# Kernel tuning notes

Hardware: AMD Instinct MI355X
Metric: run time of the kernel (lower is better)

The kernel has to match this reference:

```python
import jax, jax.numpy as jnp
import numpy as np

LMAX = 3
D_IN = 16    # sum(2l+1) for l=0..3
D_OUT = 156  # sum over the 34 CG instructions of (2*l3+1)


def _build_sparse_cg():
    """Build the concatenated sparse CG index lists (mu1, mu2, mu3) and
    coefficients, mirroring TensorProduct.__init__: loop over all
    (l1, l2, l3) paths with l3 <= LMAX, take nonzeros of the real-basis
    Wigner-3j tensor (nonzero pattern: |m1' +- m2'| == |m3'|), offset the
    indices by the per-irrep block offsets, and concatenate.
    Coefficient values are deterministic synthetic stand-ins with the
    correct sparsity structure and component-normalization scale."""
    rs = np.random.RandomState(0)
    off_in = [0, 1, 4, 9]  # block offsets for l = 0..3 (block dim 2l+1)
    mu1, mu2, mu3, vals = [], [], [], []
    off3 = 0
    for l1 in range(LMAX + 1):
        for l2 in range(LMAX + 1):
            for l3 in range(abs(l1 - l2), min(l1 + l2, LMAX) + 1):
                for m1 in range(2 * l1 + 1):
                    for m2 in range(2 * l2 + 1):
                        a, b = m1 - l1, m2 - l2
                        for m3 in range(2 * l3 + 1):
                            c = m3 - l3
                            if abs(a + b) == abs(c) or abs(a - b) == abs(c):
                                mu1.append(off_in[l1] + m1)
                                mu2.append(off_in[l2] + m2)
                                mu3.append(off3 + m3)
                                vals.append(rs.randn() / np.sqrt(2 * l3 + 1))
                off3 += 2 * l3 + 1
    assert off3 == D_OUT
    return (np.asarray(mu1, np.int32), np.asarray(mu2, np.int32),
            np.asarray(mu3, np.int32), np.asarray(vals, np.float32))


def setup_inputs() -> dict:
    key = jax.random.key(0)
    k1, k2 = jax.random.split(key)
    B, C = 1024, 128
    x = jax.random.normal(k1, (B, D_IN, C), dtype=jnp.float32)
    y = jax.random.normal(k2, (B, D_IN, C), dtype=jnp.float32)
    mu1, mu2, mu3, cg = _build_sparse_cg()
    return {
        "x": x,
        "y": y,
        "cg": jnp.asarray(cg),
        "mu1": jnp.asarray(mu1),
        "mu2": jnp.asarray(mu2),
        "mu3": jnp.asarray(mu3),
    }


def reference(x, y, cg, mu1, mu2, mu3):
    # Fused equivalent of the per-batch / per-instruction Python loops:
    # out[b, mu3[k], c] += cg[k] * x[b, mu1[k], c] * y[b, mu2[k], c]
    terms = x[:, mu1, :] * cg[None, :, None] * y[:, mu2, :]  # [B, K, C]
    out = jnp.zeros((x.shape[0], D_OUT, x.shape[2]), dtype=x.dtype)
    return out.at[:, mu3, :].add(terms)
```

## Files before the change

kernel.cpp:

```cpp
#include <hip/hip_runtime.h>
#include <utility>


#define D_IN_ 16
#define D_OUT_ 156
#define C_ 128
#define KMAX_ 2048

struct CGRows {
    int n;
    int start[D_OUT_ + 1];
    int k[KMAX_];
    int m1[KMAX_];
    int m2[KMAX_];
};

constexpr CGRows build_rows() {
    int mu1[KMAX_] = {}, mu2[KMAX_] = {}, mu3[KMAX_] = {};
    int n = 0;
    const int off_in[4] = {0, 1, 4, 9};
    int off3 = 0;
    for (int l1 = 0; l1 <= 3; ++l1) {
        for (int l2 = 0; l2 <= 3; ++l2) {
            int lo = l1 > l2 ? l1 - l2 : l2 - l1;
            int hi = (l1 + l2) < 3 ? (l1 + l2) : 3;
            for (int l3 = lo; l3 <= hi; ++l3) {
                for (int m1 = 0; m1 < 2 * l1 + 1; ++m1) {
                    for (int m2 = 0; m2 < 2 * l2 + 1; ++m2) {
                        int a = m1 - l1, b = m2 - l2;
                        for (int m3 = 0; m3 < 2 * l3 + 1; ++m3) {
                            int c = m3 - l3;
                            int s = a + b; if (s < 0) s = -s;
                            int d = a - b; if (d < 0) d = -d;
                            int e = c < 0 ? -c : c;
                            if (s == e || d == e) {
                                mu1[n] = off_in[l1] + m1;
                                mu2[n] = off_in[l2] + m2;
                                mu3[n] = off3 + m3;
                                ++n;
                            }
                        }
                    }
                }
                off3 += 2 * l3 + 1;
            }
        }
    }
    CGRows r{};
    r.n = n;
    int cnt[D_OUT_] = {};
    for (int i = 0; i < n; ++i) cnt[mu3[i]]++;
    r.start[0] = 0;
    for (int j = 0; j < D_OUT_; ++j) r.start[j + 1] = r.start[j] + cnt[j];
    int pos[D_OUT_] = {};
    for (int j = 0; j < D_OUT_; ++j) pos[j] = r.start[j];
    for (int i = 0; i < n; ++i) {
        int j = mu3[i];
        int p = pos[j]++;
        r.k[p] = i;
        r.m1[p] = mu1[i];
        r.m2[p] = mu2[i];
    }
    return r;
}

constexpr CGRows CG = build_rows();

template <int Base, int... Ts>
__device__ __forceinline__ float row_sum_impl(const float* __restrict__ cg,
                                              const float (&xv)[D_IN_],
                                              const float (&yv)[D_IN_],
                                              std::integer_sequence<int, Ts...>) {
    float s = 0.0f;
    ((s = fmaf(cg[CG.k[Base + Ts]], xv[CG.m1[Base + Ts]] * yv[CG.m2[Base + Ts]], s)), ...);
    return s;
}

template <int J>
__device__ __forceinline__ float row_sum(const float* __restrict__ cg,
                                         const float (&xv)[D_IN_],
                                         const float (&yv)[D_IN_]) {
    constexpr int base = CG.start[J];
    constexpr int nt = CG.start[J + 1] - CG.start[J];
    return row_sum_impl<base>(cg, xv, yv, std::make_integer_sequence<int, nt>{});
}

template <int... Js>
__device__ __forceinline__ void all_rows(float* __restrict__ ob,
                                         const float* __restrict__ cg,
                                         const float (&xv)[D_IN_],
                                         const float (&yv)[D_IN_],
                                         std::integer_sequence<int, Js...>) {
    ((ob[Js * C_] = row_sum<Js>(cg, xv, yv)), ...);
}

__global__ __launch_bounds__(256) void tp_cg_kernel(
    const float* __restrict__ x, const float* __restrict__ y,
    const float* __restrict__ cg, float* __restrict__ out) {
    const int c = threadIdx.x & (C_ - 1);
    const int b = (int)((blockIdx.x << 1) | (threadIdx.x >> 7));

    const float* xb = x + (size_t)b * (D_IN_ * C_) + c;
    const float* yb = y + (size_t)b * (D_IN_ * C_) + c;

    float xv[D_IN_], yv[D_IN_];
#pragma unroll
    for (int i = 0; i < D_IN_; ++i) {
        xv[i] = xb[i * C_];
        yv[i] = yb[i * C_];
    }

    float* ob = out + (size_t)b * (D_OUT_ * C_) + c;
    all_rows(ob, cg, xv, yv, std::make_integer_sequence<int, D_OUT_>{});
}

extern "C" void kernel_launch(void* const* d_in, const int* in_sizes, int n_in,
                              void* d_out, int out_size, void* d_ws, size_t ws_size,
                              hipStream_t stream) {
    const float* x  = (const float*)d_in[0];
    const float* y  = (const float*)d_in[1];
    const float* cg = (const float*)d_in[2];
    float* out = (float*)d_out;

    const int B = in_sizes[0] / (D_IN_ * C_);
    const int nblocks = (B * C_) / 256;

    tp_cg_kernel<<<nblocks, 256, 0, stream>>>(x, y, cg, out);
}
```

Baseline: 111.9 us.

## Vectorize to float2 channels, split output rows across wave halves, pre-gather CG

Each thread now handles two adjacent channels with float2 loads and stores. Each batch's output rows are split between two 64-thread halves, and each half loads only the input components its rows need. A small pre-kernel permutes the CG coefficients into row-sorted order in workspace, so the main kernel reads them contiguously instead of through indirect indices. The launch also requests two blocks per CU. The cost is an extra kernel launch, duplicated input loads across the two halves, and both branches inlined into one large kernel.

Measured after the change: 109.5 us. -2.1%, faster.

```diff
diff --git a/kernel.cpp b/kernel.cpp
--- a/kernel.cpp
+++ b/kernel.cpp
@@ -65,53 +65,97 @@
 }
 
 constexpr CGRows CG = build_rows();
+constexpr int K = CG.n;
+static_assert(K <= KMAX_, "KMAX too small");
+
+constexpr int find_split() {
+    int j = 0;
+    while (CG.start[j] < CG.n / 2) ++j;
+    return j;
+}
+constexpr int RSPLIT = find_split();
+
+constexpr unsigned need1(int j0, int j1) {
+    unsigned m = 0;
+    for (int p = CG.start[j0]; p < CG.start[j1]; ++p) m |= 1u << CG.m1[p];
+    return m;
+}
+constexpr unsigned need2(int j0, int j1) {
+    unsigned m = 0;
+    for (int p = CG.start[j0]; p < CG.start[j1]; ++p) m |= 1u << CG.m2[p];
+    return m;
+}
+
+__device__ __constant__ CGRows dCG = build_rows();
+
+__global__ void gather_cg(const float* __restrict__ cg, float* __restrict__ cgs) {
+    int i = blockIdx.x * 256 + threadIdx.x;
+    if (i < K) cgs[i] = cg[dCG.k[i]];
+}
+
+template <unsigned M, int I>
+__device__ __forceinline__ void load1(float2 (&v)[D_IN_], const float* __restrict__ base) {
+    if constexpr ((M >> I) & 1u) v[I] = *(const float2*)(base + I * C_);
+    else v[I] = make_float2(0.0f, 0.0f);
+}
+
+template <unsigned M, int... Is>
+__device__ __forceinline__ void load_masked(float2 (&v)[D_IN_], const float* __restrict__ base,
+                                            std::integer_sequence<int, Is...>) {
+    (load1<M, Is>(v, base), ...);
+}
 
 template <int Base, int... Ts>
-__device__ __forceinline__ float row_sum_impl(const float* __restrict__ cg,
-                                              const float (&xv)[D_IN_],
-                                              const float (&yv)[D_IN_],
-                                              std::integer_sequence<int, Ts...>) {
-    float s = 0.0f;
-    ((s = fmaf(cg[CG.k[Base + Ts]], xv[CG.m1[Base + Ts]] * yv[CG.m2[Base + Ts]], s)), ...);
+__device__ __forceinline__ float2 row_sum2(const float* __restrict__ cgs,
+                                           const float2 (&xv)[D_IN_],
+                                           const float2 (&yv)[D_IN_],
+                                           std::integer_sequence<int, Ts...>) {
+    float2 s = make_float2(0.0f, 0.0f);
+    (((s.x = fmaf(cgs[Base + Ts], xv[CG.m1[Base + Ts]].x * yv[CG.m2[Base + Ts]].x, s.x)),
+      (s.y = fmaf(cgs[Base + Ts], xv[CG.m1[Base + Ts]].y * yv[CG.m2[Base + Ts]].y, s.y))), ...);
     return s;
 }
 
 template <int J>
-__device__ __forceinline__ float row_sum(const float* __restrict__ cg,
-                                         const float (&xv)[D_IN_],
-                                         const float (&yv)[D_IN_]) {
+__device__ __forceinline__ void store_row(float* __restrict__ ob, const float* __restrict__ cgs,
+                                          const float2 (&xv)[D_IN_], const float2 (&yv)[D_IN_]) {
     constexpr int base = CG.start[J];
     constexpr int nt = CG.start[J + 1] - CG.start[J];
-    return row_sum_impl<base>(cg, xv, yv, std::make_integer_sequence<int, nt>{});
+    float2 s = row_sum2<base>(cgs, xv, yv, std::make_integer_sequence<int, nt>{});
+    *(float2*)(ob + J * C_) = s;
 }
 
-template <int... Js>
-__device__ __forceinline__ void all_rows(float* __restrict__ ob,
-                                         const float* __restrict__ cg,
-                                         const float (&xv)[D_IN_],
-                                         const float (&yv)[D_IN_],
-                                         std::integer_sequence<int, Js...>) {
-    ((ob[Js * C_] = row_sum<Js>(cg, xv, yv)), ...);
+template <int J0, int... Js>
+__device__ __forceinline__ void rows_range(float* __restrict__ ob, const float* __restrict__ cgs,
+                                           const float2 (&xv)[D_IN_], const float2 (&yv)[D_IN_],
+                                           std::integer_sequence<int, Js...>) {
+    (store_row<J0 + Js>(ob, cgs, xv, yv), ...);
 }
 
-__global__ __launch_bounds__(256) void tp_cg_kernel(
+__global__ __launch_bounds__(256, 2) void tp_cg_kernel(
     const float* __restrict__ x, const float* __restrict__ y,
-    const float* __restrict__ cg, float* __restrict__ out) {
-    const int c = threadIdx.x & (C_ - 1);
-    const int b = (int)((blockIdx.x << 1) | (threadIdx.x >> 7));
+    const float* __restrict__ cgs, float* __restrict__ out) {
+    const int tid = (int)threadIdx.x;
+    const int c2 = tid & 63;
+    const int half = (tid >> 6) & 1;
+    const int b = (int)((blockIdx.x << 1) | (tid >> 7));
 
-    const float* xb = x + (size_t)b * (D_IN_ * C_) + c;
-    const float* yb = y + (size_t)b * (D_IN_ * C_) + c;
+    const float* xb = x + (size_t)b * (D_IN_ * C_) + c2 * 2;
+    const float* yb = y + (size_t)b * (D_IN_ * C_) + c2 * 2;
+    float* ob = out + (size_t)b * (D_OUT_ * C_) + c2 * 2;
 
-    float xv[D_IN_], yv[D_IN_];
-#pragma unroll
-    for (int i = 0; i < D_IN_; ++i) {
-        xv[i] = xb[i * C_];
-        yv[i] = yb[i * C_];
+    float2 xv[D_IN_], yv[D_IN_];
+    if (half == 0) {
+        constexpr unsigned m1 = need1(0, RSPLIT), m2 = need2(0, RSPLIT);
+        load_masked<m1>(xv, xb, std::make_integer_sequence<int, D_IN_>{});
+        load_masked<m2>(yv, yb, std::make_integer_sequence<int, D_IN_>{});
+        rows_range<0>(ob, cgs, xv, yv, std::make_integer_sequence<int, RSPLIT>{});
+    } else {
+        constexpr unsigned m1 = need1(RSPLIT, D_OUT_), m2 = need2(RSPLIT, D_OUT_);
+        load_masked<m1>(xv, xb, std::make_integer_sequence<int, D_IN_>{});
+        load_masked<m2>(yv, yb, std::make_integer_sequence<int, D_IN_>{});
+        rows_range<RSPLIT>(ob, cgs, xv, yv, std::make_integer_sequence<int, D_OUT_ - RSPLIT>{});
     }
-
-    float* ob = out + (size_t)b * (D_OUT_ * C_) + c;
-    all_rows(ob, cg, xv, yv, std::make_integer_sequence<int, D_OUT_>{});
 }
 
 extern "C" void kernel_launch(void* const* d_in, const int* in_sizes, int n_in,
@@ -121,9 +165,12 @@
     const float* y  = (const float*)d_in[1];
     const float* cg = (const float*)d_in[2];
     float* out = (float*)d_out;
+    float* cgs = (float*)d_ws;
 
     const int B = in_sizes[0] / (D_IN_ * C_);
-    const int nblocks = (B * C_) / 256;
 
-    tp_cg_kernel<<<nblocks, 256, 0, stream>>>(x, y, cg, out);
+    gather_cg<<<(K + 255) / 256, 256, 0, stream>>>(cg, cgs);
+
+    const int nblocks = B / 2;
+    tp_cg_kernel<<<nblocks, 256, 0, stream>>>(x, y, cgs, out);
 }
```

## Split output rows across thread halves by octants, one block per batch

Applied to the files above, without the earlier changes.

Before, each thread computed all 156 output rows for one (batch, channel). Now each block handles a single batch, and its two 128-thread halves each compute four of eight octants of rows, which are balanced by term count. The octant order is rotated by batch index to spread the store pattern, and launch bounds request 4 blocks per CU. This doubles the grid and halves per-thread serial work to improve latency hiding, at the cost of every thread loading the full x/y vectors twice per batch and a runtime switch over octant code.

Result: slower. 294.2 us (+163.0%).

```diff
diff --git a/kernel.cpp b/kernel.cpp
--- a/kernel.cpp
+++ b/kernel.cpp
@@ -65,53 +65,87 @@
 }
 
 constexpr CGRows CG = build_rows();
+constexpr int K = CG.n;
+static_assert(K <= KMAX_, "KMAX too small");
+
+constexpr int findo(int i) {
+    int target = (CG.n * i) / 8;
+    int j = 0;
+    while (CG.start[j] < target) ++j;
+    return j;
+}
+constexpr int OBND[9] = {0, findo(1), findo(2), findo(3), findo(4),
+                         findo(5), findo(6), findo(7), D_OUT_};
+
+template <int... Is>
+__device__ __forceinline__ void load_all(float (&v)[D_IN_], const float* __restrict__ base,
+                                         std::integer_sequence<int, Is...>) {
+    ((v[Is] = base[Is * C_]), ...);
+}
 
 template <int Base, int... Ts>
-__device__ __forceinline__ float row_sum_impl(const float* __restrict__ cg,
-                                              const float (&xv)[D_IN_],
-                                              const float (&yv)[D_IN_],
-                                              std::integer_sequence<int, Ts...>) {
+__device__ __forceinline__ float row_sum(const float* __restrict__ cg,
+                                         const float (&xv)[D_IN_],
+                                         const float (&yv)[D_IN_],
+                                         std::integer_sequence<int, Ts...>) {
     float s = 0.0f;
     ((s = fmaf(cg[CG.k[Base + Ts]], xv[CG.m1[Base + Ts]] * yv[CG.m2[Base + Ts]], s)), ...);
     return s;
 }
 
 template <int J>
-__device__ __forceinline__ float row_sum(const float* __restrict__ cg,
-                                         const float (&xv)[D_IN_],
-                                         const float (&yv)[D_IN_]) {
+__device__ __forceinline__ void store_row(float* __restrict__ ob, const float* __restrict__ cg,
+                                          const float (&xv)[D_IN_], const float (&yv)[D_IN_]) {
     constexpr int base = CG.start[J];
     constexpr int nt = CG.start[J + 1] - CG.start[J];
-    return row_sum_impl<base>(cg, xv, yv, std::make_integer_sequence<int, nt>{});
+    ob[J * C_] = row_sum<base>(cg, xv, yv, std::make_integer_sequence<int, nt>{});
 }
 
-template <int... Js>
-__device__ __forceinline__ void all_rows(float* __restrict__ ob,
-                                         const float* __restrict__ cg,
-                                         const float (&xv)[D_IN_],
-                                         const float (&yv)[D_IN_],
-                                         std::integer_sequence<int, Js...>) {
-    ((ob[Js * C_] = row_sum<Js>(cg, xv, yv)), ...);
+template <int J0, int... Js>
+__device__ __forceinline__ void rows_range(float* __restrict__ ob, const float* __restrict__ cg,
+                                           const float (&xv)[D_IN_], const float (&yv)[D_IN_],
+                                           std::integer_sequence<int, Js...>) {
+    (store_row<J0 + Js>(ob, cg, xv, yv), ...);
 }
 
-__global__ __launch_bounds__(256) void tp_cg_kernel(
+template <int O>
+__device__ __forceinline__ void do_octant(float* __restrict__ ob, const float* __restrict__ cg,
+                                          const float (&xv)[D_IN_], const float (&yv)[D_IN_]) {
+    rows_range<OBND[O]>(ob, cg, xv, yv,
+                        std::make_integer_sequence<int, OBND[O + 1] - OBND[O]>{});
+}
+
+__global__ __launch_bounds__(256, 4) void tp_cg_kernel(
     const float* __restrict__ x, const float* __restrict__ y,
     const float* __restrict__ cg, float* __restrict__ out) {
-    const int c = threadIdx.x & (C_ - 1);
-    const int b = (int)((blockIdx.x << 1) | (threadIdx.x >> 7));
+    const int tid = (int)threadIdx.x;
+    const int c = tid & (C_ - 1);
+    const int qhalf = tid >> 7;
+    const int b = (int)blockIdx.x;
 
     const float* xb = x + (size_t)b * (D_IN_ * C_) + c;
     const float* yb = y + (size_t)b * (D_IN_ * C_) + c;
+    float* ob = out + (size_t)b * (D_OUT_ * C_) + c;
 
     float xv[D_IN_], yv[D_IN_];
-#pragma unroll
-    for (int i = 0; i < D_IN_; ++i) {
-        xv[i] = xb[i * C_];
-        yv[i] = yb[i * C_];
+    load_all(xv, xb, std::make_integer_sequence<int, D_IN_>{});
+    load_all(yv, yb, std::make_integer_sequence<int, D_IN_>{});
+
+#pragma unroll 1
+    for (int i = 0; i < 4; ++i) {
+        const int p = (i + b) & 3;
+        const int oct = (p << 1) | qhalf;
+        switch (oct) {
+            case 0: do_octant<0>(ob, cg, xv, yv); break;
+            case 1: do_octant<1>(ob, cg, xv, yv); break;
+            case 2: do_octant<2>(ob, cg, xv, yv); break;
+            case 3: do_octant<3>(ob, cg, xv, yv); break;
+            case 4: do_octant<4>(ob, cg, xv, yv); break;
+            case 5: do_octant<5>(ob, cg, xv, yv); break;
+            case 6: do_octant<6>(ob, cg, xv, yv); break;
+            default: do_octant<7>(ob, cg, xv, yv); break;
+        }
     }
-
-    float* ob = out + (size_t)b * (D_OUT_ * C_) + c;
-    all_rows(ob, cg, xv, yv, std::make_integer_sequence<int, D_OUT_>{});
 }
 
 extern "C" void kernel_launch(void* const* d_in, const int* in_sizes, int n_in,
@@ -123,7 +157,6 @@
     float* out = (float*)d_out;
 
     const int B = in_sizes[0] / (D_IN_ * C_);
-    const int nblocks = (B * C_) / 256;
 
-    tp_cg_kernel<<<nblocks, 256, 0, stream>>>(x, y, cg, out);
+    tp_cg_kernel<<<B, 256, 0, stream>>>(x, y, cg, out);
 }
```
